# Kernel tuning notes

Measured on AMD Instinct MI355X. Metric: run time of the kernel, lower is better.

## Reference

```python
import jax, jax.numpy as jnp
import numpy as np

D = 768      # num_hiddens (hardcoded by dense1/dense2/ln in the source)
H = 12       # num_heads
NEG = -1000000.0
EPS = 1e-5


def setup_inputs() -> dict:
    key = jax.random.key(0)
    ks = jax.random.split(key, 14)
    B, Lq, Lk = 8, 1024, 1024
    s = 0.02
    return {
        "queries": jax.random.normal(ks[0], (B, Lq, D), dtype=jnp.float32),
        "keys":    jax.random.normal(ks[1], (B, Lk, D), dtype=jnp.float32),
        "values":  jax.random.normal(ks[2], (B, Lk, D), dtype=jnp.float32),
        # binary padding masks; count_nonzero along axis 1 gives valid lens
        "mask_1": jax.random.randint(ks[3], (B, Lk), 0, 2, dtype=jnp.int32),
        "mask_2": jax.random.randint(ks[4], (B, Lq), 0, 2, dtype=jnp.int32),
        # projection weights stored as [in, out] (torch Linear is y = x @ W.T)
        "Wq": jax.random.normal(ks[5], (D, D), dtype=jnp.float32) * s,
        "Wk": jax.random.normal(ks[6], (D, D), dtype=jnp.float32) * s,
        "Wv": jax.random.normal(ks[7], (D, D), dtype=jnp.float32) * s,
        "Wo": jax.random.normal(ks[8], (D, D), dtype=jnp.float32) * s,
        "d1_w": jax.random.normal(ks[9], (D, D), dtype=jnp.float32) * s,
        "d1_b": jnp.zeros((D,), dtype=jnp.float32),
        "d2_w": jax.random.normal(ks[10], (D, D), dtype=jnp.float32) * s,
        "d2_b": jnp.zeros((D,), dtype=jnp.float32),
        "ln_g": jnp.ones((D,), dtype=jnp.float32),
        "ln_b": jnp.zeros((D,), dtype=jnp.float32),
    }


def _cross_att(queries, keys, values, mask_1, mask_2,
               Wq, Wk, Wv, Wo, d1_w, d1_b, d2_w, d2_b, ln_g, ln_b):
    B, Lq, _ = queries.shape
    Lk = keys.shape[1]
    hd = D // H
    # project + split heads: [B, H, L, hd]
    q = (queries @ Wq).reshape(B, Lq, H, hd).transpose(0, 2, 1, 3)
    k = (keys    @ Wk).reshape(B, Lk, H, hd).transpose(0, 2, 1, 3)
    v = (values  @ Wv).reshape(B, Lk, H, hd).transpose(0, 2, 1, 3)
    scores = jnp.einsum('bhqd,bhkd->bhqk', q, k) / jnp.sqrt(jnp.float32(hd))
    # dual-axis prefix mask from nonzero counts
    vl1 = jnp.sum(mask_1 != 0, axis=1)  # [B], masks key axis
    vl2 = jnp.sum(mask_2 != 0, axis=1)  # [B], masks query axis
    col_ok = jnp.arange(Lk)[None, None, None, :] < vl1[:, None, None, None]
    row_ok = jnp.arange(Lq)[None, None, :, None] < vl2[:, None, None, None]
    scores = jnp.where(col_ok & row_ok, scores, NEG)
    attn = jax.nn.softmax(scores, axis=-1)
    out = jnp.einsum('bhqk,bhkd->bhqd', attn, v)
    out = out.transpose(0, 2, 1, 3).reshape(B, Lq, D)
    mha = out @ Wo
    ffn = jax.nn.relu(mha @ d1_w + d1_b) @ d2_w + d2_b
    x = ffn + mha  # dropout is identity in eval
    mu = jnp.mean(x, axis=-1, keepdims=True)
    var = jnp.mean(jnp.square(x - mu), axis=-1, keepdims=True)
    return (x - mu) / jnp.sqrt(var + EPS) * ln_g + ln_b


def reference(queries, keys, values, mask_1, mask_2,
              Wq, Wk, Wv, Wo, d1_w, d1_b, d2_w, d2_b, ln_g, ln_b):
    return _cross_att(queries, keys, values, mask_1, mask_2,
                      Wq, Wk, Wv, Wo, d1_w, d1_b, d2_w, d2_b, ln_g, ln_b)
```

## Files before the change

### kernel.cpp

```cpp
#include <hip/hip_runtime.h>
#include <hip/hip_bf16.h>
#include <type_traits>

#define DM   768
#define NH   12
#define HD   64
#define BATCH 8
#define SEQ  1024
#define NROWS (BATCH * SEQ)

typedef short bf16x8 __attribute__((ext_vector_type(8)));
typedef float f32x4 __attribute__((ext_vector_type(4)));

__device__ inline unsigned short f2b(float x) {
    union { float f; unsigned int u; } v; v.f = x;
    unsigned int r = v.u + 0x7FFFu + ((v.u >> 16) & 1u);
    return (unsigned short)(r >> 16);
}
__device__ inline float b2f(unsigned short u) {
    union { float f; unsigned int x; } v; v.x = ((unsigned int)u) << 16;
    return v.f;
}

__device__ inline void gld16(const unsigned short* g, unsigned short* l) {
    __builtin_amdgcn_global_load_lds(
        (const __attribute__((address_space(1))) unsigned int*)g,
        (__attribute__((address_space(3))) unsigned int*)l, 16, 0, 0);
}

__global__ __launch_bounds__(256) void lens_kernel(const int* __restrict__ m1,
                                                   const int* __restrict__ m2,
                                                   int* __restrict__ lens) {
    __shared__ int red[256];
    const int bid = blockIdx.x;
    const int b = bid & 7;
    const int* m = (bid < 8) ? m1 : m2;
    const int t = threadIdx.x;
    int cnt = 0;
    for (int i = t; i < SEQ; i += 256) cnt += (m[b * SEQ + i] != 0) ? 1 : 0;
    red[t] = cnt;
    __syncthreads();
    for (int off = 128; off > 0; off >>= 1) {
        if (t < off) red[t] += red[t + off];
        __syncthreads();
    }
    if (t == 0) lens[bid] = red[0];
}

__global__ __launch_bounds__(256) void cvt_wt(const float* __restrict__ w0,
                                              const float* __restrict__ w1,
                                              const float* __restrict__ w2,
                                              const float* __restrict__ w3,
                                              const float* __restrict__ w4,
                                              const float* __restrict__ w5,
                                              unsigned short* __restrict__ wt) {
    __shared__ float tile[32][33];
    const int z = blockIdx.z;
    const float* W = (z == 0) ? w0 : (z == 1) ? w1 : (z == 2) ? w2
                   : (z == 3) ? w3 : (z == 4) ? w4 : w5;
    unsigned short* Wt = wt + (size_t)z * DM * DM;
    const int n0 = blockIdx.x * 32;
    const int k0 = blockIdx.y * 32;
    const int tx = threadIdx.x & 31;
    const int ty = threadIdx.x >> 5;
#pragma unroll
    for (int r = 0; r < 4; ++r)
        tile[ty + 8 * r][tx] = W[(size_t)(k0 + ty + 8 * r) * DM + n0 + tx];
    __syncthreads();
#pragma unroll
    for (int r = 0; r < 4; ++r)
        Wt[(size_t)(n0 + ty + 8 * r) * DM + k0 + tx] = f2b(tile[tx][ty + 8 * r]);
}

__global__ __launch_bounds__(256) void qkv_gemm(const float* __restrict__ a0,
                                                const float* __restrict__ a1,
                                                const float* __restrict__ a2,
                                                const unsigned short* __restrict__ wt,
                                                unsigned short* __restrict__ c0,
                                                unsigned short* __restrict__ c1,
                                                unsigned short* __restrict__ c2) {
    __shared__ __align__(16) unsigned short As[128][32];
    __shared__ __align__(16) unsigned short Ws[128][32];

    const int t = threadIdx.x;
    const int g = blockIdx.y / 6;
    const int m0 = blockIdx.x * 128;
    const int n0 = (blockIdx.y % 6) * 128;
    const float* A = (g == 0) ? a0 : (g == 1) ? a1 : a2;
    const unsigned short* Wt = wt + (size_t)g * DM * DM;
    unsigned short* C = (g == 0) ? c0 : (g == 1) ? c1 : c2;

    const int w = t >> 6, lane = t & 63;
    const int quad = lane >> 4, l16 = lane & 15;
    const int wm = w & 1, wn = w >> 1;
    const int srow = 16 * w + (lane >> 2);
    const int scol = 8 * (lane & 3);
    const int ar = t >> 1;
    const int ac = (t & 1) * 16;

    f32x4 acc[4][4];
#pragma unroll
    for (int i = 0; i < 4; ++i)
#pragma unroll
        for (int j = 0; j < 4; ++j) acc[i][j] = (f32x4){0.f, 0.f, 0.f, 0.f};

    for (int k0 = 0; k0 < DM; k0 += 32) {
#pragma unroll
        for (int j = 0; j < 2; ++j)
            gld16(&Wt[(size_t)(n0 + srow + 64 * j) * DM + k0 + scol],
                  &Ws[16 * w + 64 * j][0]);
        {
            const float* src = &A[(size_t)(m0 + ar) * DM + k0 + ac];
            float4 f0 = ((const float4*)src)[0];
            float4 f1 = ((const float4*)src)[1];
            float4 f2 = ((const float4*)src)[2];
            float4 f3 = ((const float4*)src)[3];
            union { uint4 u; unsigned short s[8]; } p0, p1;
            p0.s[0] = f2b(f0.x); p0.s[1] = f2b(f0.y); p0.s[2] = f2b(f0.z); p0.s[3] = f2b(f0.w);
            p0.s[4] = f2b(f1.x); p0.s[5] = f2b(f1.y); p0.s[6] = f2b(f1.z); p0.s[7] = f2b(f1.w);
            p1.s[0] = f2b(f2.x); p1.s[1] = f2b(f2.y); p1.s[2] = f2b(f2.z); p1.s[3] = f2b(f2.w);
            p1.s[4] = f2b(f3.x); p1.s[5] = f2b(f3.y); p1.s[6] = f2b(f3.z); p1.s[7] = f2b(f3.w);
            *(uint4*)&As[ar][ac] = p0.u;
            *(uint4*)&As[ar][ac + 8] = p1.u;
        }
        __syncthreads();

        bf16x8 av[4], bv[4];
#pragma unroll
        for (int i = 0; i < 4; ++i)
            av[i] = *(const bf16x8*)&As[wm * 64 + 16 * i + l16][quad * 8];
#pragma unroll
        for (int i = 0; i < 4; ++i)
            bv[i] = *(const bf16x8*)&Ws[wn * 64 + 16 * i + l16][quad * 8];
#pragma unroll
        for (int i = 0; i < 4; ++i)
#pragma unroll
            for (int j = 0; j < 4; ++j)
                acc[i][j] = __builtin_amdgcn_mfma_f32_16x16x32_bf16(av[i], bv[j], acc[i][j], 0, 0, 0);
        __syncthreads();
    }

#pragma unroll
    for (int i = 0; i < 4; ++i)
#pragma unroll
        for (int j = 0; j < 4; ++j) {
            const int gn = n0 + wn * 64 + 16 * j + l16;
#pragma unroll
            for (int r = 0; r < 4; ++r) {
                const int gm = m0 + wm * 64 + 16 * i + quad * 4 + r;
                C[(size_t)gm * DM + gn] = f2b(acc[i][j][r]);
            }
        }
}

template <typename CT>
__global__ __launch_bounds__(256) void gemm_bf(const unsigned short* __restrict__ A,
                                               const unsigned short* __restrict__ Wt,
                                               CT* __restrict__ C,
                                               const float* __restrict__ bias,
                                               const unsigned short* __restrict__ res,
                                               int relu) {
    __shared__ __align__(16) unsigned short As[128][32];
    __shared__ __align__(16) unsigned short Ws[128][32];

    const int t = threadIdx.x;
    const int m0 = blockIdx.x * 128;
    const int n0 = blockIdx.y * 128;
    const int w = t >> 6, lane = t & 63;
    const int quad = lane >> 4, l16 = lane & 15;
    const int wm = w & 1, wn = w >> 1;
    const int srow = 16 * w + (lane >> 2);
    const int scol = 8 * (lane & 3);

    f32x4 acc[4][4];
#pragma unroll
    for (int i = 0; i < 4; ++i)
#pragma unroll
        for (int j = 0; j < 4; ++j) acc[i][j] = (f32x4){0.f, 0.f, 0.f, 0.f};

    for (int k0 = 0; k0 < DM; k0 += 32) {
#pragma unroll
        for (int j = 0; j < 2; ++j) {
            gld16(&A[(size_t)(m0 + srow + 64 * j) * DM + k0 + scol],
                  &As[16 * w + 64 * j][0]);
            gld16(&Wt[(size_t)(n0 + srow + 64 * j) * DM + k0 + scol],
                  &Ws[16 * w + 64 * j][0]);
        }
        __syncthreads();

        bf16x8 av[4], bv[4];
#pragma unroll
        for (int i = 0; i < 4; ++i)
            av[i] = *(const bf16x8*)&As[wm * 64 + 16 * i + l16][quad * 8];
#pragma unroll
        for (int i = 0; i < 4; ++i)
            bv[i] = *(const bf16x8*)&Ws[wn * 64 + 16 * i + l16][quad * 8];
#pragma unroll
        for (int i = 0; i < 4; ++i)
#pragma unroll
            for (int j = 0; j < 4; ++j)
                acc[i][j] = __builtin_amdgcn_mfma_f32_16x16x32_bf16(av[i], bv[j], acc[i][j], 0, 0, 0);
        __syncthreads();
    }

#pragma unroll
    for (int i = 0; i < 4; ++i)
#pragma unroll
        for (int j = 0; j < 4; ++j) {
            const int gn = n0 + wn * 64 + 16 * j + l16;
            const float badd = bias ? bias[gn] : 0.0f;
#pragma unroll
            for (int r = 0; r < 4; ++r) {
                const int gm = m0 + wm * 64 + 16 * i + quad * 4 + r;
                float cv = acc[i][j][r] + badd;
                if (relu) cv = fmaxf(cv, 0.0f);
                if (res) cv += b2f(res[(size_t)gm * DM + gn]);
                if constexpr (std::is_same<CT, float>::value) {
                    C[(size_t)gm * DM + gn] = cv;
                } else {
                    C[(size_t)gm * DM + gn] = f2b(cv);
                }
            }
        }
}

__global__ __launch_bounds__(256) void attn_mfma(const unsigned short* Q,
                                                 const unsigned short* __restrict__ K,
                                                 const unsigned short* __restrict__ V,
                                                 unsigned short* O,
                                                 const int* __restrict__ lens) {
    __shared__ __align__(16) unsigned short Ks[64][72];
    __shared__ __align__(16) unsigned short Vt[64][72];
    __shared__ __align__(16) unsigned short Ps[4][16][72];

    const int t = threadIdx.x;
    const int bid = blockIdx.x;
    const int q0 = (bid & 15) * 64;
    const int h = (bid >> 4) % NH;
    const int b = bid / (16 * NH);
    const int vl1 = lens[b];
    const int vl2 = lens[8 + b];
    const int wid = t >> 6;
    const int lane = t & 63;
    const int quad = lane >> 4;
    const int l16 = lane & 15;

    bf16x8 qa0, qa1;
    {
        const unsigned short* qp =
            &Q[(size_t)(b * SEQ + q0 + 16 * wid + l16) * DM + h * HD + quad * 8];
        qa0 = *(const bf16x8*)qp;
        qa1 = *(const bf16x8*)(qp + 32);
    }

    f32x4 o[4];
#pragma unroll
    for (int ct = 0; ct < 4; ++ct) o[ct] = (f32x4){0.f, 0.f, 0.f, 0.f};
    float suml[4];
    bool rbad[4];
#pragma unroll
    for (int r = 0; r < 4; ++r) {
        suml[r] = 0.0f;
        rbad[r] = ((q0 + 16 * wid + quad * 4 + r) >= vl2) || (vl1 == 0);
    }

    const int kkr = t >> 3;
    const int khc = (t & 7) * 8;
    const unsigned short* kbase = &K[(size_t)(b * SEQ) * DM + h * HD];
    const unsigned short* vbase = &V[(size_t)(b * SEQ) * DM + h * HD];

    uint4 kr0 = *(const uint4*)&kbase[(size_t)kkr * DM + khc];
    uint4 kr1 = *(const uint4*)&kbase[(size_t)(kkr + 32) * DM + khc];
    uint4 vr0 = *(const uint4*)&vbase[(size_t)lane * DM + wid * 16];
    uint4 vr1 = *(const uint4*)&vbase[(size_t)lane * DM + wid * 16 + 8];

    const int k2 = l16 >> 2;

    for (int tile = 0; tile < 16; ++tile) {
        const int c0 = tile * 64;
        *(uint4*)&Ks[kkr][khc] = kr0;
        *(uint4*)&Ks[kkr + 32][khc] = kr1;
        {
            union { uint4 u; unsigned short s[8]; } va, vb;
            va.u = vr0; vb.u = vr1;
#pragma unroll
            for (int j = 0; j < 8; ++j) Vt[wid * 16 + j][lane] = va.s[j];
#pragma unroll
            for (int j = 0; j < 8; ++j) Vt[wid * 16 + 8 + j][lane] = vb.s[j];
        }
        __syncthreads();

        if (tile < 15) {
            const int c1 = c0 + 64;
            kr0 = *(const uint4*)&kbase[(size_t)(c1 + kkr) * DM + khc];
            kr1 = *(const uint4*)&kbase[(size_t)(c1 + kkr + 32) * DM + khc];
            vr0 = *(const uint4*)&vbase[(size_t)(c1 + lane) * DM + wid * 16];
            vr1 = *(const uint4*)&vbase[(size_t)(c1 + lane) * DM + wid * 16 + 8];
        }

        f32x4 s[4];
#pragma unroll
        for (int ct = 0; ct < 4; ++ct) {
            f32x4 acc = (f32x4){0.f, 0.f, 0.f, 0.f};
            bf16x8 b0v = *(const bf16x8*)&Ks[16 * ct + l16][quad * 8];
            bf16x8 b1v = *(const bf16x8*)&Ks[16 * ct + l16][32 + quad * 8];
            acc = __builtin_amdgcn_mfma_f32_16x16x32_bf16(qa0, b0v, acc, 0, 0, 0);
            acc = __builtin_amdgcn_mfma_f32_16x16x32_bf16(qa1, b1v, acc, 0, 0, 0);
            s[ct] = acc;
        }
#pragma unroll
        for (int ct = 0; ct < 4; ++ct) {
            const bool kok = (c0 + 16 * ct + l16) < vl1;
#pragma unroll
            for (int r = 0; r < 4; ++r) {
                float e = __expf(s[ct][r] * 0.125f);
                float p = kok ? e : 0.0f;
                p = rbad[r] ? 1.0f : p;
                s[ct][r] = p;
                suml[r] += p;
            }
        }
#pragma unroll
        for (int ct = 0; ct < 4; ++ct) {
            const int g = 2 * ct + (l16 >> 3);
            const int c = l16 & 7;
            const int gs = (g ^ quad) * 8 + c;
#pragma unroll
            for (int r = 0; r < 4; ++r)
                Ps[wid][quad * 4 + r][gs] = f2b(s[ct][r]);
        }
        bf16x8 pa0 = *(const bf16x8*)&Ps[wid][l16][(quad ^ k2) * 8];
        bf16x8 pa1 = *(const bf16x8*)&Ps[wid][l16][((4 + quad) ^ k2) * 8];
#pragma unroll
        for (int ct = 0; ct < 4; ++ct) {
            bf16x8 vb0 = *(const bf16x8*)&Vt[16 * ct + l16][quad * 8];
            bf16x8 vb1 = *(const bf16x8*)&Vt[16 * ct + l16][32 + quad * 8];
            o[ct] = __builtin_amdgcn_mfma_f32_16x16x32_bf16(pa0, vb0, o[ct], 0, 0, 0);
            o[ct] = __builtin_amdgcn_mfma_f32_16x16x32_bf16(pa1, vb1, o[ct], 0, 0, 0);
        }
        __syncthreads();
    }

#pragma unroll
    for (int d = 1; d < 16; d <<= 1) {
#pragma unroll
        for (int r = 0; r < 4; ++r) suml[r] += __shfl_xor(suml[r], d, 64);
    }
#pragma unroll
    for (int r = 0; r < 4; ++r) {
        float inv = 1.0f / suml[r];
        const size_t row = (size_t)(b * SEQ + q0 + 16 * wid + quad * 4 + r);
#pragma unroll
        for (int ct = 0; ct < 4; ++ct) {
            O[row * DM + h * HD + 16 * ct + l16] = f2b(o[ct][r] * inv);
        }
    }
}

__global__ __launch_bounds__(256) void ln_kernel(float* __restrict__ X,
                                                 const float* __restrict__ g,
                                                 const float* __restrict__ bvec) {
    __shared__ float red[256];
    const int row = blockIdx.x;
    const int t = threadIdx.x;
    float* xr = X + (size_t)row * DM;
    float x0 = xr[t];
    float x1 = xr[t + 256];
    float x2 = xr[t + 512];
    red[t] = x0 + x1 + x2;
    __syncthreads();
    for (int off = 128; off > 0; off >>= 1) {
        if (t < off) red[t] += red[t + off];
        __syncthreads();
    }
    float mu = red[0] * (1.0f / 768.0f);
    __syncthreads();
    float d0 = x0 - mu, d1 = x1 - mu, d2 = x2 - mu;
    red[t] = d0 * d0 + d1 * d1 + d2 * d2;
    __syncthreads();
    for (int off = 128; off > 0; off >>= 1) {
        if (t < off) red[t] += red[t + off];
        __syncthreads();
    }
    float rstd = rsqrtf(red[0] * (1.0f / 768.0f) + 1e-5f);
    xr[t]       = d0 * rstd * g[t]       + bvec[t];
    xr[t + 256] = d1 * rstd * g[t + 256] + bvec[t + 256];
    xr[t + 512] = d2 * rstd * g[t + 512] + bvec[t + 512];
}

extern "C" void kernel_launch(void* const* d_in, const int* in_sizes, int n_in,
                              void* d_out, int out_size, void* d_ws, size_t ws_size,
                              hipStream_t stream) {
    const float* queries = (const float*)d_in[0];
    const float* keys    = (const float*)d_in[1];
    const float* values  = (const float*)d_in[2];
    const int* mask1 = (const int*)d_in[3];
    const int* mask2 = (const int*)d_in[4];
    const float* Wq  = (const float*)d_in[5];
    const float* Wk  = (const float*)d_in[6];
    const float* Wv  = (const float*)d_in[7];
    const float* Wo  = (const float*)d_in[8];
    const float* d1w = (const float*)d_in[9];
    const float* d1b = (const float*)d_in[10];
    const float* d2w = (const float*)d_in[11];
    const float* d2b = (const float*)d_in[12];
    const float* lng = (const float*)d_in[13];
    const float* lnb = (const float*)d_in[14];

    char* ws = (char*)d_ws;
    int* lens = (int*)ws;
    const size_t NB = (size_t)NROWS * DM * sizeof(unsigned short);
    unsigned short* b0 = (unsigned short*)(ws + 256);
    unsigned short* b1 = (unsigned short*)(ws + 256 + NB);
    unsigned short* b2 = (unsigned short*)(ws + 256 + 2 * NB);
    unsigned short* wt = (unsigned short*)(ws + 256 + 3 * NB);
    float* xout = (float*)d_out;

    lens_kernel<<<16, 256, 0, stream>>>(mask1, mask2, lens);
    cvt_wt<<<dim3(24, 24, 6), 256, 0, stream>>>(Wq, Wk, Wv, Wo, d1w, d2w, wt);

    qkv_gemm<<<dim3(64, 18), 256, 0, stream>>>(queries, keys, values, wt, b0, b1, b2);

    attn_mfma<<<16 * NH * BATCH, 256, 0, stream>>>(b0, b1, b2, b0, lens);

    const size_t WT = (size_t)DM * DM;
    gemm_bf<unsigned short><<<dim3(64, 6), 256, 0, stream>>>(b0, wt + 3 * WT, b1, nullptr, nullptr, 0);
    gemm_bf<unsigned short><<<dim3(64, 6), 256, 0, stream>>>(b1, wt + 4 * WT, b2, d1b, nullptr, 1);
    gemm_bf<float><<<dim3(64, 6), 256, 0, stream>>>(b2, wt + 5 * WT, xout, d2b, b1, 0);

    ln_kernel<<<NROWS, 256, 0, stream>>>(xout, lng, lnb);
}
```

Measured before the change: 361.4 us.

## Precompose Wo·d1 weights to run Wo and dense1 GEMMs concurrently; double-buffer QKV GEMM

Adds a small kernel that computes the product Wo@d1_w on device in bf16. This lets the attention output be multiplied by Wo and by the fused Wo·d1 matrix in a single launch, so mha and relu(dense1) are produced in parallel instead of by two dependent GEMMs. The QKV GEMM now double-buffers its weight tiles and prefetches the activation row segments one k-step ahead, and the A-tile shared-memory writes are swizzled. The cost is an extra 768³ weight GEMM per call and a different rounding path for the dense1 input, since it no longer goes through a bf16-rounded mha.

```diff
diff --git a/kernel.cpp b/kernel.cpp
--- a/kernel.cpp
+++ b/kernel.cpp
@@ -72,6 +72,62 @@
         Wt[(size_t)(n0 + ty + 8 * r) * DM + k0 + tx] = f2b(tile[tx][ty + 8 * r]);
 }
 
+__global__ __launch_bounds__(256) void wod1_gemm(const float* __restrict__ Wo,
+                                                 const float* __restrict__ d1w,
+                                                 unsigned short* __restrict__ out) {
+    __shared__ __align__(16) unsigned short As[64][40];
+    __shared__ __align__(16) unsigned short Bs[64][40];
+    const int t = threadIdx.x;
+    const int mb = blockIdx.x * 64;
+    const int nb = blockIdx.y * 64;
+    const int wid = t >> 6, lane = t & 63;
+    const int quad = lane >> 4, l16 = lane & 15;
+    const int bk = t >> 3, bn = (t & 7) * 8;
+    const int am = t >> 2, ak = (t & 3) * 8;
+
+    f32x4 acc[4];
+#pragma unroll
+    for (int c = 0; c < 4; ++c) acc[c] = (f32x4){0.f, 0.f, 0.f, 0.f};
+
+    for (int j0 = 0; j0 < DM; j0 += 32) {
+        {
+            const float* s = &d1w[(size_t)(j0 + bk) * DM + mb + bn];
+            float4 f0 = ((const float4*)s)[0];
+            float4 f1 = ((const float4*)s)[1];
+            As[bn + 0][bk] = f2b(f0.x); As[bn + 1][bk] = f2b(f0.y);
+            As[bn + 2][bk] = f2b(f0.z); As[bn + 3][bk] = f2b(f0.w);
+            As[bn + 4][bk] = f2b(f1.x); As[bn + 5][bk] = f2b(f1.y);
+            As[bn + 6][bk] = f2b(f1.z); As[bn + 7][bk] = f2b(f1.w);
+        }
+        {
+            const float* s = &Wo[(size_t)(nb + am) * DM + j0 + ak];
+            float4 f0 = ((const float4*)s)[0];
+            float4 f1 = ((const float4*)s)[1];
+            union { uint4 u; unsigned short h[8]; } p;
+            p.h[0] = f2b(f0.x); p.h[1] = f2b(f0.y); p.h[2] = f2b(f0.z); p.h[3] = f2b(f0.w);
+            p.h[4] = f2b(f1.x); p.h[5] = f2b(f1.y); p.h[6] = f2b(f1.z); p.h[7] = f2b(f1.w);
+            *(uint4*)&Bs[am][ak] = p.u;
+        }
+        __syncthreads();
+        bf16x8 av = *(const bf16x8*)&As[16 * wid + l16][quad * 8];
+#pragma unroll
+        for (int c = 0; c < 4; ++c) {
+            bf16x8 bv = *(const bf16x8*)&Bs[16 * c + l16][quad * 8];
+            acc[c] = __builtin_amdgcn_mfma_f32_16x16x32_bf16(av, bv, acc[c], 0, 0, 0);
+        }
+        __syncthreads();
+    }
+#pragma unroll
+    for (int c = 0; c < 4; ++c) {
+        const int col = nb + 16 * c + l16;
+#pragma unroll
+        for (int r = 0; r < 4; ++r) {
+            const int row = mb + 16 * wid + quad * 4 + r;
+            out[(size_t)row * DM + col] = f2b(acc[c][r]);
+        }
+    }
+}
+
 __global__ __launch_bounds__(256) void qkv_gemm(const float* __restrict__ a0,
                                                 const float* __restrict__ a1,
                                                 const float* __restrict__ a2,
@@ -80,7 +136,7 @@
                                                 unsigned short* __restrict__ c1,
                                                 unsigned short* __restrict__ c2) {
     __shared__ __align__(16) unsigned short As[128][32];
-    __shared__ __align__(16) unsigned short Ws[128][32];
+    __shared__ __align__(16) unsigned short Ws[2][128][32];
 
     const int t = threadIdx.x;
     const int g = blockIdx.y / 6;
@@ -96,7 +152,10 @@
     const int srow = 16 * w + (lane >> 2);
     const int scol = 8 * (lane & 3);
     const int ar = t >> 1;
-    const int ac = (t & 1) * 16;
+    const int eps = ((ar >> 1) ^ ar) & 1;
+    const int cg1 = 2 * (t & 1) + eps;
+    const int cg2 = cg1 ^ 1;
+    const float* arow = &A[(size_t)(m0 + ar) * DM];
 
     f32x4 acc[4][4];
 #pragma unroll
@@ -104,26 +163,38 @@
 #pragma unroll
         for (int j = 0; j < 4; ++j) acc[i][j] = (f32x4){0.f, 0.f, 0.f, 0.f};
 
-    for (int k0 = 0; k0 < DM; k0 += 32) {
-#pragma unroll
-        for (int j = 0; j < 2; ++j)
-            gld16(&Wt[(size_t)(n0 + srow + 64 * j) * DM + k0 + scol],
-                  &Ws[16 * w + 64 * j][0]);
+#pragma unroll
+    for (int j = 0; j < 2; ++j)
+        gld16(&Wt[(size_t)(n0 + srow + 64 * j) * DM + scol], &Ws[0][16 * w + 64 * j][0]);
+    float4 fa0 = ((const float4*)(arow + cg1 * 8))[0];
+    float4 fa1 = ((const float4*)(arow + cg1 * 8))[1];
+    float4 fb0 = ((const float4*)(arow + cg2 * 8))[0];
+    float4 fb1 = ((const float4*)(arow + cg2 * 8))[1];
+
+    for (int ks = 0; ks < 24; ++ks) {
+        const int kb = ks & 1;
         {
-            const float* src = &A[(size_t)(m0 + ar) * DM + k0 + ac];
-            float4 f0 = ((const float4*)src)[0];
-            float4 f1 = ((const float4*)src)[1];
-            float4 f2 = ((const float4*)src)[2];
-            float4 f3 = ((const float4*)src)[3];
-            union { uint4 u; unsigned short s[8]; } p0, p1;
-            p0.s[0] = f2b(f0.x); p0.s[1] = f2b(f0.y); p0.s[2] = f2b(f0.z); p0.s[3] = f2b(f0.w);
-            p0.s[4] = f2b(f1.x); p0.s[5] = f2b(f1.y); p0.s[6] = f2b(f1.z); p0.s[7] = f2b(f1.w);
-            p1.s[0] = f2b(f2.x); p1.s[1] = f2b(f2.y); p1.s[2] = f2b(f2.z); p1.s[3] = f2b(f2.w);
-            p1.s[4] = f2b(f3.x); p1.s[5] = f2b(f3.y); p1.s[6] = f2b(f3.z); p1.s[7] = f2b(f3.w);
-            *(uint4*)&As[ar][ac] = p0.u;
-            *(uint4*)&As[ar][ac + 8] = p1.u;
-        }
-        __syncthreads();
+            union { uint4 u; unsigned short s[8]; } p, q;
+            p.s[0] = f2b(fa0.x); p.s[1] = f2b(fa0.y); p.s[2] = f2b(fa0.z); p.s[3] = f2b(fa0.w);
+            p.s[4] = f2b(fa1.x); p.s[5] = f2b(fa1.y); p.s[6] = f2b(fa1.z); p.s[7] = f2b(fa1.w);
+            q.s[0] = f2b(fb0.x); q.s[1] = f2b(fb0.y); q.s[2] = f2b(fb0.z); q.s[3] = f2b(fb0.w);
+            q.s[4] = f2b(fb1.x); q.s[5] = f2b(fb1.y); q.s[6] = f2b(fb1.z); q.s[7] = f2b(fb1.w);
+            *(uint4*)&As[ar][cg1 * 8] = p.u;
+            *(uint4*)&As[ar][cg2 * 8] = q.u;
+        }
+        __syncthreads();
+
+        if (ks != 23) {
+            const int kn = (ks + 1) * 32;
+#pragma unroll
+            for (int j = 0; j < 2; ++j)
+                gld16(&Wt[(size_t)(n0 + srow + 64 * j) * DM + kn + scol],
+                      &Ws[kb ^ 1][16 * w + 64 * j][0]);
+            fa0 = ((const float4*)(arow + kn + cg1 * 8))[0];
+            fa1 = ((const float4*)(arow + kn + cg1 * 8))[1];
+            fb0 = ((const float4*)(arow + kn + cg2 * 8))[0];
+            fb1 = ((const float4*)(arow + kn + cg2 * 8))[1];
+        }
 
         bf16x8 av[4], bv[4];
 #pragma unroll
@@ -131,7 +202,7 @@
             av[i] = *(const bf16x8*)&As[wm * 64 + 16 * i + l16][quad * 8];
 #pragma unroll
         for (int i = 0; i < 4; ++i)
-            bv[i] = *(const bf16x8*)&Ws[wn * 64 + 16 * i + l16][quad * 8];
+            bv[i] = *(const bf16x8*)&Ws[kb][wn * 64 + 16 * i + l16][quad * 8];
 #pragma unroll
         for (int i = 0; i < 4; ++i)
 #pragma unroll
@@ -224,6 +295,73 @@
         }
 }
 
+__global__ __launch_bounds__(256) void gemm_mh(const unsigned short* __restrict__ A,
+                                               const unsigned short* __restrict__ wt,
+                                               unsigned short* __restrict__ cm,
+                                               unsigned short* __restrict__ ch,
+                                               const float* __restrict__ d1b) {
+    __shared__ __align__(16) unsigned short As[128][32];
+    __shared__ __align__(16) unsigned short Ws[128][32];
+
+    const int t = threadIdx.x;
+    const int unit = blockIdx.y / 6;
+    const unsigned short* Wt = wt + (size_t)(unit ? 6 : 3) * DM * DM;
+    unsigned short* C = unit ? ch : cm;
+    const int m0 = blockIdx.x * 128;
+    const int n0 = (blockIdx.y % 6) * 128;
+    const int w = t >> 6, lane = t & 63;
+    const int quad = lane >> 4, l16 = lane & 15;
+    const int wm = w & 1, wn = w >> 1;
+    const int srow = 16 * w + (lane >> 2);
+    const int scol = 8 * (lane & 3);
+
+    f32x4 acc[4][4];
+#pragma unroll
+    for (int i = 0; i < 4; ++i)
+#pragma unroll
+        for (int j = 0; j < 4; ++j) acc[i][j] = (f32x4){0.f, 0.f, 0.f, 0.f};
+
+    for (int k0 = 0; k0 < DM; k0 += 32) {
+#pragma unroll
+        for (int j = 0; j < 2; ++j) {
+            gld16(&A[(size_t)(m0 + srow + 64 * j) * DM + k0 + scol],
+                  &As[16 * w + 64 * j][0]);
+            gld16(&Wt[(size_t)(n0 + srow + 64 * j) * DM + k0 + scol],
+                  &Ws[16 * w + 64 * j][0]);
+        }
+        __syncthreads();
+
+        bf16x8 av[4], bv[4];
+#pragma unroll
+        for (int i = 0; i < 4; ++i)
+            av[i] = *(const bf16x8*)&As[wm * 64 + 16 * i + l16][quad * 8];
+#pragma unroll
+        for (int i = 0; i < 4; ++i)
+            bv[i] = *(const bf16x8*)&Ws[wn * 64 + 16 * i + l16][quad * 8];
+#pragma unroll
+        for (int i = 0; i < 4; ++i)
+#pragma unroll
+            for (int j = 0; j < 4; ++j)
+                acc[i][j] = __builtin_amdgcn_mfma_f32_16x16x32_bf16(av[i], bv[j], acc[i][j], 0, 0, 0);
+        __syncthreads();
+    }
+
+#pragma unroll
+    for (int i = 0; i < 4; ++i)
+#pragma unroll
+        for (int j = 0; j < 4; ++j) {
+            const int gn = n0 + wn * 64 + 16 * j + l16;
+            const float badd = unit ? d1b[gn] : 0.0f;
+#pragma unroll
+            for (int r = 0; r < 4; ++r) {
+                const int gm = m0 + wm * 64 + 16 * i + quad * 4 + r;
+                float cv = acc[i][j][r] + badd;
+                if (unit) cv = fmaxf(cv, 0.0f);
+                C[(size_t)gm * DM + gn] = f2b(cv);
+            }
+        }
+}
+
 __global__ __launch_bounds__(256) void attn_mfma(const unsigned short* Q,
                                                  const unsigned short* __restrict__ K,
                                                  const unsigned short* __restrict__ V,
@@ -322,9 +460,9 @@
         }
 #pragma unroll
         for (int ct = 0; ct < 4; ++ct) {
-            const int g = 2 * ct + (l16 >> 3);
+            const int gidx = 2 * ct + (l16 >> 3);
             const int c = l16 & 7;
-            const int gs = (g ^ quad) * 8 + c;
+            const int gs = (gidx ^ quad) * 8 + c;
 #pragma unroll
             for (int r = 0; r < 4; ++r)
                 Ps[wid][quad * 4 + r][gs] = f2b(s[ct][r]);
@@ -415,17 +553,18 @@
     unsigned short* b2 = (unsigned short*)(ws + 256 + 2 * NB);
     unsigned short* wt = (unsigned short*)(ws + 256 + 3 * NB);
     float* xout = (float*)d_out;
+    const size_t WT = (size_t)DM * DM;
 
     lens_kernel<<<16, 256, 0, stream>>>(mask1, mask2, lens);
     cvt_wt<<<dim3(24, 24, 6), 256, 0, stream>>>(Wq, Wk, Wv, Wo, d1w, d2w, wt);
+    wod1_gemm<<<dim3(12, 12), 256, 0, stream>>>(Wo, d1w, wt + 6 * WT);
 
     qkv_gemm<<<dim3(64, 18), 256, 0, stream>>>(queries, keys, values, wt, b0, b1, b2);
 
     attn_mfma<<<16 * NH * BATCH, 256, 0, stream>>>(b0, b1, b2, b0, lens);
 
-    const size_t WT = (size_t)DM * DM;
-    gemm_bf<unsigned short><<<dim3(64, 6), 256, 0, stream>>>(b0, wt + 3 * WT, b1, nullptr, nullptr, 0);
-    gemm_bf<unsigned short><<<dim3(64, 6), 256, 0, stream>>>(b1, wt + 4 * WT, b2, d1b, nullptr, 1);
+    gemm_mh<<<dim3(64, 12), 256, 0, stream>>>(b0, wt, b1, b2, d1b);
+
     gemm_bf<float><<<dim3(64, 6), 256, 0, stream>>>(b2, wt + 5 * WT, xout, d2b, b1, 0);
 
     ln_kernel<<<NROWS, 256, 0, stream>>>(xout, lng, lnb);
```

Result: no change. 366.2 us (+1.3%).
